# Kernel tuning notes

Measured on AMD Instinct MI355X. Metric: run time of the kernel, lower is better.

## Reference

```python
import jax, jax.numpy as jnp
import numpy as np

N_NODES = 50000
N_EDGES = 800000
IN_C, HID_C, OUT_C = 128, 96, 64
BN_EPS = 1e-5


def setup_inputs() -> dict:
    key = jax.random.key(0)
    ks = jax.random.split(key, 12)
    x = jax.random.normal(ks[0], (N_NODES, IN_C), dtype=jnp.float32)
    edge_weight = jax.random.uniform(ks[1], (N_EDGES,), dtype=jnp.float32)
    row = jax.random.randint(ks[2], (N_EDGES,), 0, N_NODES, dtype=jnp.int32)
    col = jax.random.randint(ks[3], (N_EDGES,), 0, N_NODES, dtype=jnp.int32)
    s = 0.05
    W1 = jax.random.normal(ks[4], (IN_C, HID_C), dtype=jnp.float32) * s
    b1 = jnp.zeros((HID_C,), dtype=jnp.float32)
    W2 = jax.random.normal(ks[5], (HID_C, HID_C), dtype=jnp.float32) * s
    b2 = jnp.zeros((HID_C,), dtype=jnp.float32)
    W3 = jax.random.normal(ks[6], (HID_C, OUT_C), dtype=jnp.float32) * s
    b3 = jnp.zeros((OUT_C,), dtype=jnp.float32)
    g1 = jnp.ones((HID_C,), dtype=jnp.float32)
    be1 = jnp.zeros((HID_C,), dtype=jnp.float32)
    g2 = jnp.ones((HID_C,), dtype=jnp.float32)
    be2 = jnp.zeros((HID_C,), dtype=jnp.float32)
    return {"x": x, "edge_weight": edge_weight, "row": row, "col": col,
            "W1": W1, "b1": b1, "W2": W2, "b2": b2, "W3": W3, "b3": b3,
            "g1": g1, "be1": be1, "g2": g2, "be2": be2}


def _gcn_conv(h, edge_weight, row, col, W, b):
    # GCNConv: adj_norm @ (h @ W) + b, adj in COO with normalized edge_weight
    h = h @ W  # [N, d_out]
    msg = edge_weight[:, None] * h[col]  # gather + scale: [E, d_out]
    agg = jax.ops.segment_sum(msg, row, num_segments=N_NODES)  # scatter-add
    return agg + b


def _batch_norm(h, gamma, beta):
    # BatchNorm1d (training-mode batch statistics, biased variance)
    mean = jnp.mean(h, axis=0)
    var = jnp.var(h, axis=0)
    return (h - mean) * jax.lax.rsqrt(var + BN_EPS) * gamma + beta


def reference(x, edge_weight, row, col, W1, b1, W2, b2, W3, b3, g1, be1, g2, be2):
    h = _gcn_conv(x, edge_weight, row, col, W1, b1)
    h = jax.nn.relu(_batch_norm(h, g1, be1))  # dropout is identity in eval
    h = _gcn_conv(h, edge_weight, row, col, W2, b2)
    h = jax.nn.relu(_batch_norm(h, g2, be2))
    h = _gcn_conv(h, edge_weight, row, col, W3, b3)
    return jax.nn.log_softmax(h, axis=-1)
```

## Files before the change

### kernel.cpp

```cpp
#include <hip/hip_runtime.h>
#include <hip/hip_bf16.h>
#include <math.h>

#define N_NODES 50000
#define N_EDGES 800000
#define IN_C 128
#define HID_C 96
#define OUT_C 64
#define BN_EPS 1e-5f

#define ELL_SHIFT 6
#define ELL_CAP   64

#define NGRP 8
#define GRP_ROWS ((N_NODES + NGRP - 1) / NGRP)

#define EW_SCALE 65535.0f
#define EW_INV   (1.0f / 65535.0f)

#define ST_SLICES 4

typedef __attribute__((ext_vector_type(8))) short short8;
typedef __attribute__((ext_vector_type(4))) float f32x4;

static __device__ __forceinline__ unsigned short f2b(float f) {
    __hip_bfloat16 b = __float2bfloat16(f);
    return *reinterpret_cast<unsigned short*>(&b);
}
static __device__ __forceinline__ float b2f(unsigned short u) {
    return __uint_as_float((unsigned)u << 16);
}
static __device__ __forceinline__ unsigned pack2(float a, float b) {
    return (unsigned)f2b(a) | ((unsigned)f2b(b) << 16);
}

#define FMA8(B, V, W)                                          \
    acc[(B) + 0] += (W) * __uint_as_float((V).x << 16);        \
    acc[(B) + 1] += (W) * __uint_as_float((V).x & 0xffff0000u);\
    acc[(B) + 2] += (W) * __uint_as_float((V).y << 16);        \
    acc[(B) + 3] += (W) * __uint_as_float((V).y & 0xffff0000u);\
    acc[(B) + 4] += (W) * __uint_as_float((V).z << 16);        \
    acc[(B) + 5] += (W) * __uint_as_float((V).z & 0xffff0000u);\
    acc[(B) + 6] += (W) * __uint_as_float((V).w << 16);        \
    acc[(B) + 7] += (W) * __uint_as_float((V).w & 0xffff0000u);

#define FMA4(B, V, W)                                          \
    acc[(B) + 0] += (W) * __uint_as_float((V).x << 16);        \
    acc[(B) + 1] += (W) * __uint_as_float((V).x & 0xffff0000u);\
    acc[(B) + 2] += (W) * __uint_as_float((V).y << 16);        \
    acc[(B) + 3] += (W) * __uint_as_float((V).y & 0xffff0000u);

__global__ void prep_all(const float* __restrict__ W1, const float* __restrict__ W2,
                         const float* __restrict__ W3,
                         unsigned short* __restrict__ Wt1,
                         unsigned short* __restrict__ Wt2,
                         unsigned short* __restrict__ Wt3,
                         int* __restrict__ cnt, float* __restrict__ stats) {
    int i = blockIdx.x * blockDim.x + threadIdx.x;
    const int n1 = IN_C * HID_C, n2 = HID_C * HID_C, n3 = HID_C * OUT_C;
    if (i < n1) {
        int j = i / IN_C, k = i % IN_C;
        Wt1[i] = f2b(W1[k * HID_C + j]);
    } else if (i < n1 + n2) {
        int t = i - n1, j = t / HID_C, k = t % HID_C;
        Wt2[t] = f2b(W2[k * HID_C + j]);
    } else if (i < n1 + n2 + n3) {
        int t = i - n1 - n2, j = t / HID_C, k = t % HID_C;
        Wt3[t] = f2b(W3[k * OUT_C + j]);
    }
    if (i < N_NODES) cnt[i] = 0;
    if (i < 2 * ST_SLICES * 2 * HID_C) stats[i] = 0.f;
}

__global__ __launch_bounds__(256)
void fill_ell(const int* __restrict__ row, const int* __restrict__ col,
              const float* __restrict__ ew, int* __restrict__ cnt,
              unsigned int* __restrict__ pairs) {
    int g = blockIdx.x & (NGRP - 1);
    int e = (blockIdx.x >> 3) * 256 + threadIdx.x;
    if (e >= N_EDGES) return;
    int r = row[e];
    int lo = g * GRP_ROWS;
    if ((unsigned)(r - lo) >= (unsigned)GRP_ROWS) return;
    int slot = atomicAdd(&cnt[r], 1);
    if (slot < ELL_CAP) {
        unsigned wq = (unsigned)(ew[e] * EW_SCALE + 0.5f);
        pairs[((size_t)r << ELL_SHIFT) + slot] = (wq << 16) | (unsigned)col[e];
    }
}

template <int K, int J, bool APPLY, bool XBF16>
__global__ __launch_bounds__(256)
void gemm_mfma(const void* __restrict__ xin,
               const unsigned short* __restrict__ Wt,
               const float* __restrict__ stats,
               const float* __restrict__ gamma,
               const float* __restrict__ beta,
               unsigned short* __restrict__ h, int N) {
    constexpr int MT = 64;
    constexpr int SK = K + 8;
    constexpr int NT = J / 16;
    __shared__ unsigned short Xs[MT * SK];
    __shared__ unsigned short Ws[J * SK];
    __shared__ float scsh_s[APPLY ? 2 * K : 2];

    int tid = threadIdx.x;
    int tileBase = blockIdx.x * MT;

    if (APPLY) {
        if (tid < K) {
            float s = 0.f, sq = 0.f;
#pragma unroll
            for (int sl = 0; sl < ST_SLICES; ++sl) {
                s  += stats[sl * 2 * K + tid];
                sq += stats[sl * 2 * K + K + tid];
            }
            const float invN = 1.f / N_NODES;
            float mean = s * invN;
            float var = sq * invN - mean * mean;
            float sc = gamma[tid] * rsqrtf(var + BN_EPS);
            scsh_s[tid] = sc;
            scsh_s[K + tid] = beta[tid] - mean * sc;
        }
        __syncthreads();
    }

    if (XBF16) {
        const unsigned short* xb = (const unsigned short*)xin;
        for (int i = tid; i < MT * (K / 8); i += 256) {
            int node = i / (K / 8), kq = i % (K / 8);
            int gn = min(tileBase + node, N - 1);
            const unsigned short* src = xb + (size_t)gn * K + kq * 8;
            ushort4 u0 = *(const ushort4*)(src);
            ushort4 u1 = *(const ushort4*)(src + 4);
            if (APPLY) {
                int kb = kq * 8;
                float v0 = fmaxf(b2f(u0.x) * scsh_s[kb + 0] + scsh_s[K + kb + 0], 0.f);
                float v1 = fmaxf(b2f(u0.y) * scsh_s[kb + 1] + scsh_s[K + kb + 1], 0.f);
                float v2 = fmaxf(b2f(u0.z) * scsh_s[kb + 2] + scsh_s[K + kb + 2], 0.f);
                float v3 = fmaxf(b2f(u0.w) * scsh_s[kb + 3] + scsh_s[K + kb + 3], 0.f);
                float v4 = fmaxf(b2f(u1.x) * scsh_s[kb + 4] + scsh_s[K + kb + 4], 0.f);
                float v5 = fmaxf(b2f(u1.y) * scsh_s[kb + 5] + scsh_s[K + kb + 5], 0.f);
                float v6 = fmaxf(b2f(u1.z) * scsh_s[kb + 6] + scsh_s[K + kb + 6], 0.f);
                float v7 = fmaxf(b2f(u1.w) * scsh_s[kb + 7] + scsh_s[K + kb + 7], 0.f);
                u0 = make_ushort4(f2b(v0), f2b(v1), f2b(v2), f2b(v3));
                u1 = make_ushort4(f2b(v4), f2b(v5), f2b(v6), f2b(v7));
            }
            *(ushort4*)&Xs[node * SK + kq * 8] = u0;
            *(ushort4*)&Xs[node * SK + kq * 8 + 4] = u1;
        }
    } else {
        const float* xf = (const float*)xin;
        for (int i = tid; i < MT * (K / 4); i += 256) {
            int node = i / (K / 4), kq = i % (K / 4);
            int gn = min(tileBase + node, N - 1);
            float4 v = *(const float4*)(xf + (size_t)gn * K + kq * 4);
            ushort4 o = make_ushort4(f2b(v.x), f2b(v.y), f2b(v.z), f2b(v.w));
            *(ushort4*)&Xs[node * SK + kq * 4] = o;
        }
    }
    for (int i = tid; i < J * (K / 4); i += 256) {
        int j = i / (K / 4), kq = i % (K / 4);
        *(ushort4*)&Ws[j * SK + kq * 4] =
            *(const ushort4*)(Wt + (size_t)j * K + kq * 4);
    }
    __syncthreads();

    int lane = tid & 63;
    int w = tid >> 6;
    int m16 = lane & 15;
    int quad = lane >> 4;

    f32x4 acc[NT];
#pragma unroll
    for (int nt = 0; nt < NT; ++nt) acc[nt] = (f32x4){0.f, 0.f, 0.f, 0.f};

    const unsigned short* xrow = &Xs[(w * 16 + m16) * SK];
#pragma unroll
    for (int k0 = 0; k0 < K; k0 += 32) {
        short8 a = *(const short8*)(xrow + k0 + quad * 8);
#pragma unroll
        for (int nt = 0; nt < NT; ++nt) {
            short8 b = *(const short8*)&Ws[(nt * 16 + m16) * SK + k0 + quad * 8];
            acc[nt] = __builtin_amdgcn_mfma_f32_16x16x32_bf16(a, b, acc[nt], 0, 0, 0);
        }
    }

#pragma unroll
    for (int nt = 0; nt < NT; ++nt) {
#pragma unroll
        for (int r = 0; r < 4; ++r) {
            int node = tileBase + w * 16 + quad * 4 + r;
            if (node < N)
                h[(size_t)node * J + nt * 16 + m16] = f2b(acc[nt][r]);
        }
    }
}

__global__ __launch_bounds__(256, 6)
void agg96(const unsigned short* __restrict__ h,
           const int* __restrict__ cnt,
           const unsigned int* __restrict__ pairs,
           unsigned short* __restrict__ outb,
           float* __restrict__ stats) {
    constexpr int D = HID_C, C = 12;
    int tid = threadIdx.x;
    int q = tid & 7;
    int nloc = tid >> 3;
    int n = blockIdx.x * 32 + nloc;
    bool valid = n < N_NODES;
    int nn = valid ? n : N_NODES - 1;
    int end = valid ? min(cnt[nn], ELL_CAP) : 0;
    const unsigned* ep = pairs + ((size_t)nn << ELL_SHIFT);
    const int cbase = q * C;

    float acc[C];
#pragma unroll
    for (int c = 0; c < C; ++c) acc[c] = 0.f;

    int i = 0;
    for (; i + 5 < end; i += 6) {
        uint2 pa = *(const uint2*)(ep + i);
        uint2 pb = *(const uint2*)(ep + i + 2);
        uint2 pc = *(const uint2*)(ep + i + 4);
        float w0 = (float)(pa.x >> 16) * EW_INV;
        float w1 = (float)(pa.y >> 16) * EW_INV;
        float w2 = (float)(pb.x >> 16) * EW_INV;
        float w3 = (float)(pb.y >> 16) * EW_INV;
        float w4 = (float)(pc.x >> 16) * EW_INV;
        float w5 = (float)(pc.y >> 16) * EW_INV;
        const unsigned short* r0 = h + (size_t)(pa.x & 0xFFFFu) * D + cbase;
        const unsigned short* r1 = h + (size_t)(pa.y & 0xFFFFu) * D + cbase;
        const unsigned short* r2 = h + (size_t)(pb.x & 0xFFFFu) * D + cbase;
        const unsigned short* r3 = h + (size_t)(pb.y & 0xFFFFu) * D + cbase;
        const unsigned short* r4 = h + (size_t)(pc.x & 0xFFFFu) * D + cbase;
        const unsigned short* r5 = h + (size_t)(pc.y & 0xFFFFu) * D + cbase;
        uint2 a0 = *(const uint2*)(r0), a1 = *(const uint2*)(r0 + 4), a2 = *(const uint2*)(r0 + 8);
        uint2 b0 = *(const uint2*)(r1), b1 = *(const uint2*)(r1 + 4), b2 = *(const uint2*)(r1 + 8);
        uint2 c0 = *(const uint2*)(r2), c1 = *(const uint2*)(r2 + 4), c2 = *(const uint2*)(r2 + 8);
        uint2 d0 = *(const uint2*)(r3), d1 = *(const uint2*)(r3 + 4), d2 = *(const uint2*)(r3 + 8);
        uint2 e0 = *(const uint2*)(r4), e1 = *(const uint2*)(r4 + 4), e2 = *(const uint2*)(r4 + 8);
        uint2 f0 = *(const uint2*)(r5), f1 = *(const uint2*)(r5 + 4), f2 = *(const uint2*)(r5 + 8);
        FMA4(0, a0, w0) FMA4(4, a1, w0) FMA4(8, a2, w0)
        FMA4(0, b0, w1) FMA4(4, b1, w1) FMA4(8, b2, w1)
        FMA4(0, c0, w2) FMA4(4, c1, w2) FMA4(8, c2, w2)
        FMA4(0, d0, w3) FMA4(4, d1, w3) FMA4(8, d2, w3)
        FMA4(0, e0, w4) FMA4(4, e1, w4) FMA4(8, e2, w4)
        FMA4(0, f0, w5) FMA4(4, f1, w5) FMA4(8, f2, w5)
    }
    for (; i < end; ++i) {
        unsigned p = ep[i];
        float w = (float)(p >> 16) * EW_INV;
        const unsigned short* r0 = h + (size_t)(p & 0xFFFFu) * D + cbase;
        uint2 a0 = *(const uint2*)(r0), a1 = *(const uint2*)(r0 + 4), a2 = *(const uint2*)(r0 + 8);
        FMA4(0, a0, w) FMA4(4, a1, w) FMA4(8, a2, w)
    }

#pragma unroll
    for (int c = 0; c < C; ++c) acc[c] = b2f(f2b(acc[c]));

    if (valid) {
        unsigned short* dst = outb + (size_t)n * D + cbase;
        uint2 o0, o1, o2;
        o0.x = pack2(acc[0], acc[1]);   o0.y = pack2(acc[2], acc[3]);
        o1.x = pack2(acc[4], acc[5]);   o1.y = pack2(acc[6], acc[7]);
        o2.x = pack2(acc[8], acc[9]);   o2.y = pack2(acc[10], acc[11]);
        *(uint2*)(dst) = o0; *(uint2*)(dst + 4) = o1; *(uint2*)(dst + 8) = o2;
    }

    __shared__ float shS[4 * 8 * C];
    __shared__ float shQ[4 * 8 * C];
    int lane = tid & 63, wv = tid >> 6;
#pragma unroll
    for (int c = 0; c < C; ++c) {
        float s = acc[c];
        float sq = s * s;
        s  += __shfl_xor(s, 8);  sq += __shfl_xor(sq, 8);
        s  += __shfl_xor(s, 16); sq += __shfl_xor(sq, 16);
        s  += __shfl_xor(s, 32); sq += __shfl_xor(sq, 32);
        if (lane < 8) { shS[(wv * 8 + lane) * C + c] = s;
                        shQ[(wv * 8 + lane) * C + c] = sq; }
    }
    __syncthreads();
    if (tid < D) {
        int qq = tid / C, cl = tid % C;
        float S = 0.f, Q = 0.f;
#pragma unroll
        for (int w2 = 0; w2 < 4; ++w2) {
            S += shS[(w2 * 8 + qq) * C + cl];
            Q += shQ[(w2 * 8 + qq) * C + cl];
        }
        int sl = blockIdx.x & (ST_SLICES - 1);
        atomicAdd(&stats[sl * 2 * D + tid], S);
        atomicAdd(&stats[sl * 2 * D + D + tid], Q);
    }
}

__global__ __launch_bounds__(256, 6)
void agg64_lsm(const unsigned short* __restrict__ h,
               const int* __restrict__ cnt,
               const unsigned int* __restrict__ pairs,
               float* __restrict__ outf,
               const float* __restrict__ b3) {
    constexpr int D = OUT_C, C = 8;
    int tid = threadIdx.x;
    int q = tid & 7;
    int nloc = tid >> 3;
    int n = blockIdx.x * 32 + nloc;
    bool valid = n < N_NODES;
    int nn = valid ? n : N_NODES - 1;
    int end = valid ? min(cnt[nn], ELL_CAP) : 0;
    const unsigned* ep = pairs + ((size_t)nn << ELL_SHIFT);
    const int cbase = q * C;

    float acc[C];
#pragma unroll
    for (int c = 0; c < C; ++c) acc[c] = 0.f;

    int i = 0;
    for (; i + 5 < end; i += 6) {
        uint2 pa = *(const uint2*)(ep + i);
        uint2 pb = *(const uint2*)(ep + i + 2);
        uint2 pc = *(const uint2*)(ep + i + 4);
        float w0 = (float)(pa.x >> 16) * EW_INV;
        float w1 = (float)(pa.y >> 16) * EW_INV;
        float w2 = (float)(pb.x >> 16) * EW_INV;
        float w3 = (float)(pb.y >> 16) * EW_INV;
        float w4 = (float)(pc.x >> 16) * EW_INV;
        float w5 = (float)(pc.y >> 16) * EW_INV;
        uint4 v0 = *(const uint4*)(h + (size_t)(pa.x & 0xFFFFu) * D + cbase);
        uint4 v1 = *(const uint4*)(h + (size_t)(pa.y & 0xFFFFu) * D + cbase);
        uint4 v2 = *(const uint4*)(h + (size_t)(pb.x & 0xFFFFu) * D + cbase);
        uint4 v3 = *(const uint4*)(h + (size_t)(pb.y & 0xFFFFu) * D + cbase);
        uint4 v4 = *(const uint4*)(h + (size_t)(pc.x & 0xFFFFu) * D + cbase);
        uint4 v5 = *(const uint4*)(h + (size_t)(pc.y & 0xFFFFu) * D + cbase);
        FMA8(0, v0, w0)
        FMA8(0, v1, w1)
        FMA8(0, v2, w2)
        FMA8(0, v3, w3)
        FMA8(0, v4, w4)
        FMA8(0, v5, w5)
    }
    for (; i < end; ++i) {
        unsigned p = ep[i];
        float w = (float)(p >> 16) * EW_INV;
        uint4 v = *(const uint4*)(h + (size_t)(p & 0xFFFFu) * D + cbase);
        FMA8(0, v, w)
    }

    float v[C];
#pragma unroll
    for (int c = 0; c < C; ++c) v[c] = acc[c] + b3[cbase + c];
    float m = v[0];
#pragma unroll
    for (int c = 1; c < C; ++c) m = fmaxf(m, v[c]);
    m = fmaxf(m, __shfl_xor(m, 1));
    m = fmaxf(m, __shfl_xor(m, 2));
    m = fmaxf(m, __shfl_xor(m, 4));
    float s = 0.f;
#pragma unroll
    for (int c = 0; c < C; ++c) s += expf(v[c] - m);
    s += __shfl_xor(s, 1);
    s += __shfl_xor(s, 2);
    s += __shfl_xor(s, 4);
    float l = m + logf(s);
    if (valid) {
        float4 o0 = make_float4(v[0] - l, v[1] - l, v[2] - l, v[3] - l);
        float4 o1 = make_float4(v[4] - l, v[5] - l, v[6] - l, v[7] - l);
        float* dst = outf + (size_t)n * D + cbase;
        *(float4*)(dst) = o0;
        *(float4*)(dst + 4) = o1;
    }
}

extern "C" void kernel_launch(void* const* d_in, const int* in_sizes, int n_in,
                              void* d_out, int out_size, void* d_ws, size_t ws_size,
                              hipStream_t stream) {
    const float* x   = (const float*)d_in[0];
    const float* ew  = (const float*)d_in[1];
    const int*   row = (const int*)d_in[2];
    const int*   col = (const int*)d_in[3];
    const float* W1  = (const float*)d_in[4];
    const float* W2  = (const float*)d_in[6];
    const float* W3  = (const float*)d_in[8];
    const float* b3  = (const float*)d_in[9];
    const float* g1  = (const float*)d_in[10];
    const float* be1 = (const float*)d_in[11];
    const float* g2  = (const float*)d_in[12];
    const float* be2 = (const float*)d_in[13];
    float* out = (float*)d_out;

    unsigned short* B      = (unsigned short*)d_ws;
    unsigned short* A      = B + (size_t)N_NODES * HID_C;
    unsigned short* Wt1    = A + (size_t)N_NODES * HID_C;
    unsigned short* Wt2    = Wt1 + IN_C * HID_C;
    unsigned short* Wt3    = Wt2 + HID_C * HID_C;
    unsigned int*   pairs  = (unsigned int*)(Wt3 + HID_C * OUT_C);
    int*            cnt    = (int*)(pairs + ((size_t)N_NODES << ELL_SHIFT));
    float*          stats1 = (float*)(cnt + N_NODES);
    float*          stats2 = stats1 + ST_SLICES * 2 * HID_C;

    const int T = 256;
    const int gridE  = (N_EDGES + T - 1) / T;
    const int gridG  = (N_NODES + 63) / 64;
    const int gridA  = (N_NODES + 31) / 32;
    const int gridP  = (N_NODES + T - 1) / T;

    prep_all<<<gridP, T, 0, stream>>>(W1, W2, W3, Wt1, Wt2, Wt3, cnt, stats1);
    fill_ell<<<gridE * NGRP, T, 0, stream>>>(row, col, ew, cnt, pairs);

    gemm_mfma<IN_C, HID_C, false, false><<<gridG, T, 0, stream>>>(
        x, Wt1, nullptr, nullptr, nullptr, A, N_NODES);
    agg96<<<gridA, T, 0, stream>>>(A, cnt, pairs, B, stats1);

    gemm_mfma<HID_C, HID_C, true, true><<<gridG, T, 0, stream>>>(
        B, Wt2, stats1, g1, be1, A, N_NODES);
    agg96<<<gridA, T, 0, stream>>>(A, cnt, pairs, B, stats2);

    gemm_mfma<HID_C, OUT_C, true, true><<<gridG, T, 0, stream>>>(
        B, Wt3, stats2, g2, be2, A, N_NODES);
    agg64_lsm<<<gridA, T, 0, stream>>>(A, cnt, pairs, out, b3);
}
```

Measured before the change: 256.6 us.

## Remap agg96 to 12 lanes per node with 16-byte gathers and LDS-atomic stats

```diff
diff --git a/kernel.cpp b/kernel.cpp
--- a/kernel.cpp
+++ b/kernel.cpp
@@ -43,12 +43,6 @@
     acc[(B) + 5] += (W) * __uint_as_float((V).z & 0xffff0000u);\
     acc[(B) + 6] += (W) * __uint_as_float((V).w << 16);        \
     acc[(B) + 7] += (W) * __uint_as_float((V).w & 0xffff0000u);
-
-#define FMA4(B, V, W)                                          \
-    acc[(B) + 0] += (W) * __uint_as_float((V).x << 16);        \
-    acc[(B) + 1] += (W) * __uint_as_float((V).x & 0xffff0000u);\
-    acc[(B) + 2] += (W) * __uint_as_float((V).y << 16);        \
-    acc[(B) + 3] += (W) * __uint_as_float((V).y & 0xffff0000u);
 
 __global__ void prep_all(const float* __restrict__ W1, const float* __restrict__ W2,
                          const float* __restrict__ W3,
@@ -197,102 +191,80 @@
     }
 }
 
-__global__ __launch_bounds__(256, 6)
+__global__ __launch_bounds__(256, 8)
 void agg96(const unsigned short* __restrict__ h,
            const int* __restrict__ cnt,
            const unsigned int* __restrict__ pairs,
            unsigned short* __restrict__ outb,
            float* __restrict__ stats) {
-    constexpr int D = HID_C, C = 12;
+    constexpr int D = HID_C;
     int tid = threadIdx.x;
-    int q = tid & 7;
-    int nloc = tid >> 3;
-    int n = blockIdx.x * 32 + nloc;
-    bool valid = n < N_NODES;
-    int nn = valid ? n : N_NODES - 1;
+    int wv = tid >> 6, lane = tid & 63;
+    int nl = lane / 12;
+    int q = lane - nl * 12;
+    int n = blockIdx.x * 20 + wv * 5 + nl;
+    bool valid = (nl < 5) && (n < N_NODES);
+    int nn = valid ? n : 0;
     int end = valid ? min(cnt[nn], ELL_CAP) : 0;
     const unsigned* ep = pairs + ((size_t)nn << ELL_SHIFT);
-    const int cbase = q * C;
-
-    float acc[C];
-#pragma unroll
-    for (int c = 0; c < C; ++c) acc[c] = 0.f;
+    const int cbase = q * 8;
+
+    float acc[8];
+#pragma unroll
+    for (int c = 0; c < 8; ++c) acc[c] = 0.f;
 
     int i = 0;
-    for (; i + 5 < end; i += 6) {
+    for (; i + 3 < end; i += 4) {
         uint2 pa = *(const uint2*)(ep + i);
         uint2 pb = *(const uint2*)(ep + i + 2);
-        uint2 pc = *(const uint2*)(ep + i + 4);
         float w0 = (float)(pa.x >> 16) * EW_INV;
         float w1 = (float)(pa.y >> 16) * EW_INV;
         float w2 = (float)(pb.x >> 16) * EW_INV;
         float w3 = (float)(pb.y >> 16) * EW_INV;
-        float w4 = (float)(pc.x >> 16) * EW_INV;
-        float w5 = (float)(pc.y >> 16) * EW_INV;
-        const unsigned short* r0 = h + (size_t)(pa.x & 0xFFFFu) * D + cbase;
-        const unsigned short* r1 = h + (size_t)(pa.y & 0xFFFFu) * D + cbase;
-        const unsigned short* r2 = h + (size_t)(pb.x & 0xFFFFu) * D + cbase;
-        const unsigned short* r3 = h + (size_t)(pb.y & 0xFFFFu) * D + cbase;
-        const unsigned short* r4 = h + (size_t)(pc.x & 0xFFFFu) * D + cbase;
-        const unsigned short* r5 = h + (size_t)(pc.y & 0xFFFFu) * D + cbase;
-        uint2 a0 = *(const uint2*)(r0), a1 = *(const uint2*)(r0 + 4), a2 = *(const uint2*)(r0 + 8);
-        uint2 b0 = *(const uint2*)(r1), b1 = *(const uint2*)(r1 + 4), b2 = *(const uint2*)(r1 + 8);
-        uint2 c0 = *(const uint2*)(r2), c1 = *(const uint2*)(r2 + 4), c2 = *(const uint2*)(r2 + 8);
-        uint2 d0 = *(const uint2*)(r3), d1 = *(const uint2*)(r3 + 4), d2 = *(const uint2*)(r3 + 8);
-        uint2 e0 = *(const uint2*)(r4), e1 = *(const uint2*)(r4 + 4), e2 = *(const uint2*)(r4 + 8);
-        uint2 f0 = *(const uint2*)(r5), f1 = *(const uint2*)(r5 + 4), f2 = *(const uint2*)(r5 + 8);
-        FMA4(0, a0, w0) FMA4(4, a1, w0) FMA4(8, a2, w0)
-        FMA4(0, b0, w1) FMA4(4, b1, w1) FMA4(8, b2, w1)
-        FMA4(0, c0, w2) FMA4(4, c1, w2) FMA4(8, c2, w2)
-        FMA4(0, d0, w3) FMA4(4, d1, w3) FMA4(8, d2, w3)
-        FMA4(0, e0, w4) FMA4(4, e1, w4) FMA4(8, e2, w4)
-        FMA4(0, f0, w5) FMA4(4, f1, w5) FMA4(8, f2, w5)
+        uint4 v0 = *(const uint4*)(h + (size_t)(pa.x & 0xFFFFu) * D + cbase);
+        uint4 v1 = *(const uint4*)(h + (size_t)(pa.y & 0xFFFFu) * D + cbase);
+        uint4 v2 = *(const uint4*)(h + (size_t)(pb.x & 0xFFFFu) * D + cbase);
+        uint4 v3 = *(const uint4*)(h + (size_t)(pb.y & 0xFFFFu) * D + cbase);
+        FMA8(0, v0, w0)
+        FMA8(0, v1, w1)
+        FMA8(0, v2, w2)
+        FMA8(0, v3, w3)
     }
     for (; i < end; ++i) {
         unsigned p = ep[i];
         float w = (float)(p >> 16) * EW_INV;
-        const unsigned short* r0 = h + (size_t)(p & 0xFFFFu) * D + cbase;
-        uint2 a0 = *(const uint2*)(r0), a1 = *(const uint2*)(r0 + 4), a2 = *(const uint2*)(r0 + 8);
-        FMA4(0, a0, w) FMA4(4, a1, w) FMA4(8, a2, w)
-    }
-
-#pragma unroll
-    for (int c = 0; c < C; ++c) acc[c] = b2f(f2b(acc[c]));
+        uint4 v = *(const uint4*)(h + (size_t)(p & 0xFFFFu) * D + cbase);
+        FMA8(0, v, w)
+    }
+
+#pragma unroll
+    for (int c = 0; c < 8; ++c) acc[c] = b2f(f2b(acc[c]));
 
     if (valid) {
-        unsigned short* dst = outb + (size_t)n * D + cbase;
-        uint2 o0, o1, o2;
-        o0.x = pack2(acc[0], acc[1]);   o0.y = pack2(acc[2], acc[3]);
-        o1.x = pack2(acc[4], acc[5]);   o1.y = pack2(acc[6], acc[7]);
-        o2.x = pack2(acc[8], acc[9]);   o2.y = pack2(acc[10], acc[11]);
-        *(uint2*)(dst) = o0; *(uint2*)(dst + 4) = o1; *(uint2*)(dst + 8) = o2;
-    }
-
-    __shared__ float shS[4 * 8 * C];
-    __shared__ float shQ[4 * 8 * C];
-    int lane = tid & 63, wv = tid >> 6;
-#pragma unroll
-    for (int c = 0; c < C; ++c) {
-        float s = acc[c];
-        float sq = s * s;
-        s  += __shfl_xor(s, 8);  sq += __shfl_xor(sq, 8);
-        s  += __shfl_xor(s, 16); sq += __shfl_xor(sq, 16);
-        s  += __shfl_xor(s, 32); sq += __shfl_xor(sq, 32);
-        if (lane < 8) { shS[(wv * 8 + lane) * C + c] = s;
-                        shQ[(wv * 8 + lane) * C + c] = sq; }
+        uint4 o;
+        o.x = pack2(acc[0], acc[1]);
+        o.y = pack2(acc[2], acc[3]);
+        o.z = pack2(acc[4], acc[5]);
+        o.w = pack2(acc[6], acc[7]);
+        *(uint4*)(outb + (size_t)n * D + cbase) = o;
+    }
+
+    __shared__ float shS[D];
+    __shared__ float shQ[D];
+    if (tid < D) { shS[tid] = 0.f; shQ[tid] = 0.f; }
+    __syncthreads();
+    if (valid) {
+#pragma unroll
+        for (int c = 0; c < 8; ++c) {
+            atomicAdd(&shS[cbase + c], acc[c]);
+            atomicAdd(&shQ[cbase + c], acc[c] * acc[c]);
+        }
     }
     __syncthreads();
     if (tid < D) {
-        int qq = tid / C, cl = tid % C;
-        float S = 0.f, Q = 0.f;
-#pragma unroll
-        for (int w2 = 0; w2 < 4; ++w2) {
-            S += shS[(w2 * 8 + qq) * C + cl];
-            Q += shQ[(w2 * 8 + qq) * C + cl];
-        }
         int sl = blockIdx.x & (ST_SLICES - 1);
-        atomicAdd(&stats[sl * 2 * D + tid], S);
-        atomicAdd(&stats[sl * 2 * D + D + tid], Q);
+        atomicAdd(&stats[sl * 2 * D + tid], shS[tid]);
+        atomicAdd(&stats[sl * 2 * D + D + tid], shQ[tid]);
     }
 }
 
@@ -403,7 +375,8 @@
     const int T = 256;
     const int gridE  = (N_EDGES + T - 1) / T;
     const int gridG  = (N_NODES + 63) / 64;
-    const int gridA  = (N_NODES + 31) / 32;
+    const int gridA9 = (N_NODES + 19) / 20;
+    const int gridA6 = (N_NODES + 31) / 32;
     const int gridP  = (N_NODES + T - 1) / T;
 
     prep_all<<<gridP, T, 0, stream>>>(W1, W2, W3, Wt1, Wt2, Wt3, cnt, stats1);
@@ -411,13 +384,13 @@
 
     gemm_mfma<IN_C, HID_C, false, false><<<gridG, T, 0, stream>>>(
         x, Wt1, nullptr, nullptr, nullptr, A, N_NODES);
-    agg96<<<gridA, T, 0, stream>>>(A, cnt, pairs, B, stats1);
+    agg96<<<gridA9, T, 0, stream>>>(A, cnt, pairs, B, stats1);
 
     gemm_mfma<HID_C, HID_C, true, true><<<gridG, T, 0, stream>>>(
         B, Wt2, stats1, g1, be1, A, N_NODES);
-    agg96<<<gridA, T, 0, stream>>>(A, cnt, pairs, B, stats2);
+    agg96<<<gridA9, T, 0, stream>>>(A, cnt, pairs, B, stats2);
 
     gemm_mfma<HID_C, OUT_C, true, true><<<gridG, T, 0, stream>>>(
         B, Wt3, stats2, g2, be2, A, N_NODES);
-    agg64_lsm<<<gridA, T, 0, stream>>>(A, cnt, pairs, out, b3);
-}
+    agg64_lsm<<<gridA6, T, 0, stream>>>(A, cnt, pairs, out, b3);
+}
```

Result: slower. 322.3 us (+25.6%).
